# Performance work log

Measured on AMD Instinct MI355X. Metric: run time of the kernel, lower is better.

## Reference

```python
import jax, jax.numpy as jnp
import numpy as np

N_NODES = 100000
N_EDGES = 1600000
D_FEAT = 32


def setup_inputs() -> dict:
    key = jax.random.key(0)
    k1, k2, k3 = jax.random.split(key, 3)
    h = jax.random.normal(k1, (N_NODES, D_FEAT), dtype=jnp.float32)
    src = jax.random.randint(k2, (N_EDGES,), 0, N_NODES, dtype=jnp.int64)
    dst = jax.random.randint(k3, (N_EDGES,), 0, N_NODES, dtype=jnp.int64)
    return {"h": h, "src": src, "dst": dst}


def reference(h, src, dst):
    n = h.shape[0]
    # gather source features per edge, scatter-add into destination nodes
    msg_sum = jax.ops.segment_sum(h[src], dst, num_segments=n)  # [N, D]
    deg = jax.ops.segment_sum(jnp.ones_like(dst, dtype=h.dtype), dst, num_segments=n)  # [N]
    # mean over mailbox; nodes with no in-edges get 0 (DGL leaves them unset/zero)
    h_N = msg_sum / jnp.maximum(deg, 1.0)[:, None]
    return h_N
```

## Files before the change

kernel.cpp:

```cpp
#include <hip/hip_runtime.h>
#include <hip/hip_bf16.h>


#define D_FEAT 32

__global__ void zero_init_kernel(float* __restrict__ out, int out_n,
                                 float* __restrict__ deg, int n_nodes) {
    int total = out_n + n_nodes;
    for (int i = blockIdx.x * blockDim.x + threadIdx.x; i < total;
         i += gridDim.x * blockDim.x) {
        if (i < out_n) out[i] = 0.0f;
        else deg[i - out_n] = 0.0f;
    }
}

__global__ void scatter_kernel(const float* __restrict__ h,
                               const int* __restrict__ src,
                               const int* __restrict__ dst,
                               float* __restrict__ out,
                               float* __restrict__ deg,
                               int n_edges) {
    long long tid = (long long)blockIdx.x * blockDim.x + threadIdx.x;
    long long total = (long long)n_edges * D_FEAT;
    if (tid >= total) return;
    int e = (int)(tid >> 5);
    int d = (int)(tid & 31);
    int s = src[e];
    int t = dst[e];
    float v = h[(long long)s * D_FEAT + d];
    atomicAdd(&out[(long long)t * D_FEAT + d], v);
    if (d == 0) atomicAdd(&deg[t], 1.0f);
}

__global__ void finalize_kernel(float* __restrict__ out,
                                const float* __restrict__ deg,
                                int n_nodes) {
    int total = n_nodes * D_FEAT;
    for (int i = blockIdx.x * blockDim.x + threadIdx.x; i < total;
         i += gridDim.x * blockDim.x) {
        float dg = deg[i >> 5];
        out[i] = out[i] / fmaxf(dg, 1.0f);
    }
}

extern "C" void kernel_launch(void* const* d_in, const int* in_sizes, int n_in,
                              void* d_out, int out_size, void* d_ws, size_t ws_size,
                              hipStream_t stream) {
    const float* h  = (const float*)d_in[0];
    const int* src  = (const int*)d_in[1];
    const int* dst  = (const int*)d_in[2];
    float* out      = (float*)d_out;

    int n_nodes = in_sizes[0] / D_FEAT;
    int n_edges = in_sizes[1];

    float* deg = (float*)d_ws;

    {
        int total = n_nodes * D_FEAT + n_nodes;
        int block = 256;
        int grid  = min((total + block - 1) / block, 2048);
        zero_init_kernel<<<grid, block, 0, stream>>>(out, n_nodes * D_FEAT, deg, n_nodes);
    }

    {
        long long total = (long long)n_edges * D_FEAT;
        int block = 256;
        long long grid = (total + block - 1) / block;
        scatter_kernel<<<(int)grid, block, 0, stream>>>(h, src, dst, out, deg, n_edges);
    }

    {
        int total = n_nodes * D_FEAT;
        int block = 256;
        int grid  = min((total + block - 1) / block, 2048);
        finalize_kernel<<<grid, block, 0, stream>>>(out, deg, n_nodes);
    }
}
```

Baseline: 319.7 us.

## Build CSR by destination and gather per node instead of atomic scatter

Replaces the per-element float atomic scatter with a CSR build: count in-degrees with integer atomics, prefix-scan them into offsets, bucket the source indices by destination, then have one 32-lane group per node gather and average its incoming features. This removes 51M float atomics on the output and the separate zeroing and finalize passes. In exchange it adds five extra kernel launches and two passes of integer atomics over the edges. Summation order within a node is now nondeterministic only through bucket order. If the workspace is too small it falls back to the old path.

```diff
diff --git a/kernel.cpp b/kernel.cpp
--- a/kernel.cpp
+++ b/kernel.cpp
@@ -3,6 +3,123 @@
 
 
 #define D_FEAT 32
+#define SCAN_BLOCK 256
+#define SCAN_CHUNK 1024
+
+__global__ void zero_i32_kernel(int* __restrict__ p, int n) {
+    for (int i = blockIdx.x * blockDim.x + threadIdx.x; i < n;
+         i += gridDim.x * blockDim.x) p[i] = 0;
+}
+
+__global__ void degree_kernel(const int* __restrict__ dst, int* __restrict__ deg,
+                              int n_edges) {
+    for (int i = blockIdx.x * blockDim.x + threadIdx.x; i < n_edges;
+         i += gridDim.x * blockDim.x) {
+        atomicAdd(&deg[dst[i]], 1);
+    }
+}
+
+__global__ void scan_reduce_kernel(const int* __restrict__ deg, int n,
+                                   int* __restrict__ blocksum) {
+    __shared__ int tmp[SCAN_BLOCK];
+    int b = blockIdx.x;
+    int base = b * SCAN_CHUNK + threadIdx.x * 4;
+    int s = 0;
+    #pragma unroll
+    for (int k = 0; k < 4; ++k) {
+        int i = base + k;
+        if (i < n) s += deg[i];
+    }
+    tmp[threadIdx.x] = s;
+    __syncthreads();
+    for (int ofs = SCAN_BLOCK / 2; ofs > 0; ofs >>= 1) {
+        if (threadIdx.x < ofs) tmp[threadIdx.x] += tmp[threadIdx.x + ofs];
+        __syncthreads();
+    }
+    if (threadIdx.x == 0) blocksum[b] = tmp[0];
+}
+
+__global__ void scan_toplevel_kernel(const int* __restrict__ blocksum,
+                                     int* __restrict__ blockoff, int nb) {
+    __shared__ int tmp[SCAN_BLOCK];
+    int t = threadIdx.x;
+    int orig = (t < nb) ? blocksum[t] : 0;
+    int v = orig;
+    for (int ofs = 1; ofs < SCAN_BLOCK; ofs <<= 1) {
+        tmp[t] = v;
+        __syncthreads();
+        if (t >= ofs) v += tmp[t - ofs];
+        __syncthreads();
+    }
+    if (t < nb) blockoff[t] = v - orig;
+}
+
+__global__ void scan_final_kernel(const int* __restrict__ deg,
+                                  const int* __restrict__ blockoff,
+                                  int* __restrict__ offsets,
+                                  int* __restrict__ cursor, int n) {
+    __shared__ int tmp[SCAN_BLOCK];
+    int b = blockIdx.x, t = threadIdx.x;
+    int base = b * SCAN_CHUNK + t * 4;
+    int d[4];
+    #pragma unroll
+    for (int k = 0; k < 4; ++k) d[k] = (base + k < n) ? deg[base + k] : 0;
+    int tsum = d[0] + d[1] + d[2] + d[3];
+    int v = tsum;
+    for (int ofs = 1; ofs < SCAN_BLOCK; ofs <<= 1) {
+        tmp[t] = v;
+        __syncthreads();
+        if (t >= ofs) v += tmp[t - ofs];
+        __syncthreads();
+    }
+    int run = v - tsum + blockoff[b];
+    #pragma unroll
+    for (int k = 0; k < 4; ++k) {
+        int i = base + k;
+        if (i < n) {
+            offsets[i] = run;
+            cursor[i]  = run;
+            run += d[k];
+            if (i == n - 1) offsets[n] = run;
+        }
+    }
+}
+
+__global__ void bucket_scatter_kernel(const int* __restrict__ src,
+                                      const int* __restrict__ dst,
+                                      int* __restrict__ cursor,
+                                      int* __restrict__ srcs_sorted,
+                                      int n_edges) {
+    for (int i = blockIdx.x * blockDim.x + threadIdx.x; i < n_edges;
+         i += gridDim.x * blockDim.x) {
+        int t = dst[i];
+        int pos = atomicAdd(&cursor[t], 1);
+        srcs_sorted[pos] = src[i];
+    }
+}
+
+__global__ void gather_kernel(const float* __restrict__ h,
+                              const int* __restrict__ srcs_sorted,
+                              const int* __restrict__ offsets,
+                              float* __restrict__ out, int n_nodes) {
+    int node = blockIdx.x * (blockDim.x >> 5) + (threadIdx.x >> 5);
+    if (node >= n_nodes) return;
+    int d = threadIdx.x & 31;
+    int beg = offsets[node];
+    int end = offsets[node + 1];
+    float v = 0.0f;
+    for (int j0 = beg; j0 < end; j0 += 32) {
+        int myidx = j0 + d;
+        int s_my = (myidx < end) ? srcs_sorted[myidx] : 0;
+        int cnt = min(32, end - j0);
+        for (int k = 0; k < cnt; ++k) {
+            int s = __shfl(s_my, k, 32);
+            v += h[(size_t)s * D_FEAT + d];
+        }
+    }
+    float deg = (float)(end - beg);
+    out[(size_t)node * D_FEAT + d] = v / fmaxf(deg, 1.0f);
+}
 
 __global__ void zero_init_kernel(float* __restrict__ out, int out_n,
                                  float* __restrict__ deg, int n_nodes) {
@@ -13,67 +130,70 @@
         else deg[i - out_n] = 0.0f;
     }
 }
-
 __global__ void scatter_kernel(const float* __restrict__ h,
                                const int* __restrict__ src,
                                const int* __restrict__ dst,
                                float* __restrict__ out,
-                               float* __restrict__ deg,
-                               int n_edges) {
+                               float* __restrict__ deg, int n_edges) {
     long long tid = (long long)blockIdx.x * blockDim.x + threadIdx.x;
     long long total = (long long)n_edges * D_FEAT;
     if (tid >= total) return;
     int e = (int)(tid >> 5);
     int d = (int)(tid & 31);
-    int s = src[e];
-    int t = dst[e];
-    float v = h[(long long)s * D_FEAT + d];
-    atomicAdd(&out[(long long)t * D_FEAT + d], v);
-    if (d == 0) atomicAdd(&deg[t], 1.0f);
+    float v = h[(long long)src[e] * D_FEAT + d];
+    atomicAdd(&out[(long long)dst[e] * D_FEAT + d], v);
+    if (d == 0) atomicAdd(&deg[dst[e]], 1.0f);
 }
-
 __global__ void finalize_kernel(float* __restrict__ out,
-                                const float* __restrict__ deg,
-                                int n_nodes) {
+                                const float* __restrict__ deg, int n_nodes) {
     int total = n_nodes * D_FEAT;
     for (int i = blockIdx.x * blockDim.x + threadIdx.x; i < total;
-         i += gridDim.x * blockDim.x) {
-        float dg = deg[i >> 5];
-        out[i] = out[i] / fmaxf(dg, 1.0f);
-    }
+         i += gridDim.x * blockDim.x)
+        out[i] = out[i] / fmaxf(deg[i >> 5], 1.0f);
 }
 
 extern "C" void kernel_launch(void* const* d_in, const int* in_sizes, int n_in,
                               void* d_out, int out_size, void* d_ws, size_t ws_size,
                               hipStream_t stream) {
-    const float* h  = (const float*)d_in[0];
-    const int* src  = (const int*)d_in[1];
-    const int* dst  = (const int*)d_in[2];
-    float* out      = (float*)d_out;
+    const float* h = (const float*)d_in[0];
+    const int* src = (const int*)d_in[1];
+    const int* dst = (const int*)d_in[2];
+    float* out = (float*)d_out;
 
     int n_nodes = in_sizes[0] / D_FEAT;
     int n_edges = in_sizes[1];
+    int nb = (n_nodes + SCAN_CHUNK - 1) / SCAN_CHUNK;
 
-    float* deg = (float*)d_ws;
-
-    {
-        int total = n_nodes * D_FEAT + n_nodes;
-        int block = 256;
-        int grid  = min((total + block - 1) / block, 2048);
-        zero_init_kernel<<<grid, block, 0, stream>>>(out, n_nodes * D_FEAT, deg, n_nodes);
+    size_t need = ((size_t)3 * n_nodes + 1 + 2 * nb + n_edges) * sizeof(int);
+    if (ws_size < need || nb > SCAN_BLOCK) {
+        float* deg = (float*)d_ws;
+        int total0 = n_nodes * D_FEAT + n_nodes;
+        zero_init_kernel<<<min((total0 + 255) / 256, 2048), 256, 0, stream>>>(
+            out, n_nodes * D_FEAT, deg, n_nodes);
+        long long total = (long long)n_edges * D_FEAT;
+        scatter_kernel<<<(int)((total + 255) / 256), 256, 0, stream>>>(
+            h, src, dst, out, deg, n_edges);
+        finalize_kernel<<<min((n_nodes * D_FEAT + 255) / 256, 2048), 256, 0,
+                          stream>>>(out, deg, n_nodes);
+        return;
     }
 
-    {
-        long long total = (long long)n_edges * D_FEAT;
-        int block = 256;
-        long long grid = (total + block - 1) / block;
-        scatter_kernel<<<(int)grid, block, 0, stream>>>(h, src, dst, out, deg, n_edges);
-    }
+    int* wsI        = (int*)d_ws;
+    int* deg        = wsI;
+    int* offsets    = deg + n_nodes;
+    int* cursor     = offsets + n_nodes + 1;
+    int* blocksum   = cursor + n_nodes;
+    int* blockoff   = blocksum + nb;
+    int* srcs_sorted= blockoff + nb;
 
-    {
-        int total = n_nodes * D_FEAT;
-        int block = 256;
-        int grid  = min((total + block - 1) / block, 2048);
-        finalize_kernel<<<grid, block, 0, stream>>>(out, deg, n_nodes);
-    }
+    zero_i32_kernel<<<min((n_nodes + 255) / 256, 2048), 256, 0, stream>>>(deg, n_nodes);
+    degree_kernel<<<2048, 256, 0, stream>>>(dst, deg, n_edges);
+    scan_reduce_kernel<<<nb, SCAN_BLOCK, 0, stream>>>(deg, n_nodes, blocksum);
+    scan_toplevel_kernel<<<1, SCAN_BLOCK, 0, stream>>>(blocksum, blockoff, nb);
+    scan_final_kernel<<<nb, SCAN_BLOCK, 0, stream>>>(deg, blockoff, offsets, cursor, n_nodes);
+    bucket_scatter_kernel<<<2048, 256, 0, stream>>>(src, dst, cursor, srcs_sorted, n_edges);
+
+    int nodes_per_block = 256 / 32;
+    int grid = (n_nodes + nodes_per_block - 1) / nodes_per_block;
+    gather_kernel<<<grid, 256, 0, stream>>>(h, srcs_sorted, offsets, out, n_nodes);
 }
```

Measured after the change: 320.9 us. No clear change (+0.4%).

## Bucket edges by destination block and aggregate in shared memory

Applied to the files above, without the earlier changes.

Replaces the global-atomic scatter with a counting-sort of edges into buckets of 128 destination nodes, built with a histogram, a scan and a pack pass. Each block then accumulates its bucket's messages and degrees with shared-memory atomics and writes the normalized mean directly, which removes the zero-init and finalize passes and the contention on global atomics. Packing the local destination and the source into one int limits source ids to 17 bits. It adds four extra small kernels plus extra passes over dst, and the old path is kept as a fallback when the workspace is too small or there are too many buckets.

```diff
diff --git a/kernel.cpp b/kernel.cpp
--- a/kernel.cpp
+++ b/kernel.cpp
@@ -3,6 +3,107 @@
 
 
 #define D_FEAT 32
+#define NPB 128
+#define SHIFT 7
+#define PACK_GRID 256
+
+__global__ void zero_i32_kernel(int* __restrict__ p, int n) {
+    for (int i = blockIdx.x * blockDim.x + threadIdx.x; i < n;
+         i += gridDim.x * blockDim.x) p[i] = 0;
+}
+
+__global__ void hist_kernel(const int* __restrict__ dst, int n_edges,
+                            int* __restrict__ bucket_cnt, int nb) {
+    extern __shared__ int lbin[];
+    for (int i = threadIdx.x; i < nb; i += blockDim.x) lbin[i] = 0;
+    __syncthreads();
+    for (int i = blockIdx.x * blockDim.x + threadIdx.x; i < n_edges;
+         i += gridDim.x * blockDim.x)
+        atomicAdd(&lbin[dst[i] >> SHIFT], 1);
+    __syncthreads();
+    for (int i = threadIdx.x; i < nb; i += blockDim.x)
+        if (lbin[i]) atomicAdd(&bucket_cnt[i], lbin[i]);
+}
+
+__global__ void scan_bins_kernel(const int* __restrict__ cnt,
+                                 int* __restrict__ off,
+                                 int* __restrict__ cur, int nb) {
+    __shared__ int tmp[1024];
+    int t = threadIdx.x;
+    int orig = (t < nb) ? cnt[t] : 0;
+    int v = orig;
+    for (int o = 1; o < 1024; o <<= 1) {
+        tmp[t] = v;
+        __syncthreads();
+        if (t >= o) v += tmp[t - o];
+        __syncthreads();
+    }
+    if (t < nb) {
+        off[t] = v - orig;
+        cur[t] = v - orig;
+        if (t == nb - 1) off[nb] = v;
+    }
+}
+
+__global__ void pack_scatter_kernel(const int* __restrict__ src,
+                                    const int* __restrict__ dst, int n_edges,
+                                    int* __restrict__ bucket_cur,
+                                    int* __restrict__ packed, int nb, int epb) {
+    extern __shared__ int sh[];
+    int* lcnt = sh;
+    int* lcur = sh + nb;
+    int lo = blockIdx.x * epb;
+    int hi = min(lo + epb, n_edges);
+    for (int i = threadIdx.x; i < nb; i += blockDim.x) lcnt[i] = 0;
+    __syncthreads();
+    for (int i = lo + threadIdx.x; i < hi; i += blockDim.x)
+        atomicAdd(&lcnt[dst[i] >> SHIFT], 1);
+    __syncthreads();
+    for (int i = threadIdx.x; i < nb; i += blockDim.x) {
+        int c = lcnt[i];
+        lcur[i] = c ? atomicAdd(&bucket_cur[i], c) : 0;
+    }
+    __syncthreads();
+    for (int i = lo + threadIdx.x; i < hi; i += blockDim.x) {
+        int dd = dst[i];
+        int b = dd >> SHIFT;
+        int pos = atomicAdd(&lcur[b], 1);
+        packed[pos] = ((dd & (NPB - 1)) << 17) | src[i];
+    }
+}
+
+__global__ __launch_bounds__(256) void aggregate_kernel(
+        const float* __restrict__ h, const int* __restrict__ packed,
+        const int* __restrict__ off, float* __restrict__ out, int n_nodes) {
+    __shared__ float acc[NPB * D_FEAT];
+    __shared__ int degi[NPB];
+    int b = blockIdx.x;
+    for (int i = threadIdx.x; i < NPB * D_FEAT; i += 256) acc[i] = 0.0f;
+    for (int i = threadIdx.x; i < NPB; i += 256) degi[i] = 0;
+    __syncthreads();
+
+    int beg = off[b], end = off[b + 1];
+    int lane = threadIdx.x & 63;
+    int wid  = threadIdx.x >> 6;
+    int half = lane >> 5;
+    int d    = lane & 31;
+    for (int j = beg + wid * 2 + half; j < end; j += 8) {
+        int p  = packed[j];
+        int s  = p & 0x1FFFF;
+        int ld = p >> 17;
+        float v = h[(size_t)s * D_FEAT + d];
+        atomicAdd(&acc[ld * D_FEAT + d], v);
+        if (d == 0) atomicAdd(&degi[ld], 1);
+    }
+    __syncthreads();
+
+    size_t obase = (size_t)b * NPB * D_FEAT;
+    for (int i = threadIdx.x; i < NPB * D_FEAT; i += 256) {
+        int node = b * NPB + (i >> 5);
+        if (node < n_nodes)
+            out[obase + i] = acc[i] / fmaxf((float)degi[i >> 5], 1.0f);
+    }
+}
 
 __global__ void zero_init_kernel(float* __restrict__ out, int out_n,
                                  float* __restrict__ deg, int n_nodes) {
@@ -13,67 +114,65 @@
         else deg[i - out_n] = 0.0f;
     }
 }
-
 __global__ void scatter_kernel(const float* __restrict__ h,
                                const int* __restrict__ src,
                                const int* __restrict__ dst,
                                float* __restrict__ out,
-                               float* __restrict__ deg,
-                               int n_edges) {
+                               float* __restrict__ deg, int n_edges) {
     long long tid = (long long)blockIdx.x * blockDim.x + threadIdx.x;
     long long total = (long long)n_edges * D_FEAT;
     if (tid >= total) return;
     int e = (int)(tid >> 5);
     int d = (int)(tid & 31);
-    int s = src[e];
-    int t = dst[e];
-    float v = h[(long long)s * D_FEAT + d];
-    atomicAdd(&out[(long long)t * D_FEAT + d], v);
-    if (d == 0) atomicAdd(&deg[t], 1.0f);
+    float v = h[(long long)src[e] * D_FEAT + d];
+    atomicAdd(&out[(long long)dst[e] * D_FEAT + d], v);
+    if (d == 0) atomicAdd(&deg[dst[e]], 1.0f);
 }
-
 __global__ void finalize_kernel(float* __restrict__ out,
-                                const float* __restrict__ deg,
-                                int n_nodes) {
+                                const float* __restrict__ deg, int n_nodes) {
     int total = n_nodes * D_FEAT;
     for (int i = blockIdx.x * blockDim.x + threadIdx.x; i < total;
-         i += gridDim.x * blockDim.x) {
-        float dg = deg[i >> 5];
-        out[i] = out[i] / fmaxf(dg, 1.0f);
-    }
+         i += gridDim.x * blockDim.x)
+        out[i] = out[i] / fmaxf(deg[i >> 5], 1.0f);
 }
 
 extern "C" void kernel_launch(void* const* d_in, const int* in_sizes, int n_in,
                               void* d_out, int out_size, void* d_ws, size_t ws_size,
                               hipStream_t stream) {
-    const float* h  = (const float*)d_in[0];
-    const int* src  = (const int*)d_in[1];
-    const int* dst  = (const int*)d_in[2];
-    float* out      = (float*)d_out;
+    const float* h = (const float*)d_in[0];
+    const int* src = (const int*)d_in[1];
+    const int* dst = (const int*)d_in[2];
+    float* out = (float*)d_out;
 
     int n_nodes = in_sizes[0] / D_FEAT;
     int n_edges = in_sizes[1];
+    int nb = (n_nodes + NPB - 1) >> SHIFT;
 
-    float* deg = (float*)d_ws;
-
-    {
-        int total = n_nodes * D_FEAT + n_nodes;
-        int block = 256;
-        int grid  = min((total + block - 1) / block, 2048);
-        zero_init_kernel<<<grid, block, 0, stream>>>(out, n_nodes * D_FEAT, deg, n_nodes);
+    size_t need = ((size_t)3 * nb + 1 + (size_t)n_edges) * sizeof(int);
+    if (ws_size < need || nb > 1024) {
+        float* deg = (float*)d_ws;
+        int total0 = n_nodes * D_FEAT + n_nodes;
+        zero_init_kernel<<<min((total0 + 255) / 256, 2048), 256, 0, stream>>>(
+            out, n_nodes * D_FEAT, deg, n_nodes);
+        long long total = (long long)n_edges * D_FEAT;
+        scatter_kernel<<<(int)((total + 255) / 256), 256, 0, stream>>>(
+            h, src, dst, out, deg, n_edges);
+        finalize_kernel<<<min((n_nodes * D_FEAT + 255) / 256, 2048), 256, 0,
+                          stream>>>(out, deg, n_nodes);
+        return;
     }
 
-    {
-        long long total = (long long)n_edges * D_FEAT;
-        int block = 256;
-        long long grid = (total + block - 1) / block;
-        scatter_kernel<<<(int)grid, block, 0, stream>>>(h, src, dst, out, deg, n_edges);
-    }
+    int* wsI        = (int*)d_ws;
+    int* bucket_cnt = wsI;
+    int* bucket_off = bucket_cnt + nb;
+    int* bucket_cur = bucket_off + nb + 1;
+    int* packed     = bucket_cur + nb;
 
-    {
-        int total = n_nodes * D_FEAT;
-        int block = 256;
-        int grid  = min((total + block - 1) / block, 2048);
-        finalize_kernel<<<grid, block, 0, stream>>>(out, deg, n_nodes);
-    }
+    zero_i32_kernel<<<4, 256, 0, stream>>>(bucket_cnt, nb);
+    hist_kernel<<<256, 256, nb * sizeof(int), stream>>>(dst, n_edges, bucket_cnt, nb);
+    scan_bins_kernel<<<1, 1024, 0, stream>>>(bucket_cnt, bucket_off, bucket_cur, nb);
+    int epb = (n_edges + PACK_GRID - 1) / PACK_GRID;
+    pack_scatter_kernel<<<PACK_GRID, 256, 2 * nb * sizeof(int), stream>>>(
+        src, dst, n_edges, bucket_cur, packed, nb, epb);
+    aggregate_kernel<<<nb, 256, 0, stream>>>(h, packed, bucket_off, out, n_nodes);
 }
```

Result: slower. 484.2 us (+51.5%).
